# Kernel optimization log

Hardware: AMD Instinct MI355X
Metric: run time of the kernel (lower is better)

The kernel has to match this reference:

```python
import jax, jax.numpy as jnp
import numpy as np

E = 131072
MS, MV = 64, 32            # node/edge/out irreps: 64x0e + 32x1o (dim 160)
DIM = MS + 3 * MV
SC = 64                    # edge scalar dim
BETA = 1.6791767           # normalize2mom(silu) constant used by e3nn FullyConnectedNet
SQ3 = np.float32(np.sqrt(3.0))


def _split(x, ms, mv):
    # e3nn layout: [mul_s scalars | mul_v vectors (mul-major, xyz-minor)]
    return x[:, :ms], x[:, ms:].reshape(x.shape[0], mv, 3)


def _tp(xs, xv, ys, yv, Wss, Wvv, Wsv, Wvs):
    # uvw fully-connected tensor product of (m1s x0e + m1v x1o) with (1x0e + 1x1o),
    # component irrep normalization, 1/sqrt(fan_in) path weights.
    m1s, m1v = xs.shape[1], xv.shape[1]
    s_a = jnp.einsum('eu,uw->ew', xs * ys, Wss) / np.sqrt(m1s)              # 0e x 0e -> 0e
    dot = jnp.einsum('eui,ei->eu', xv, yv) / SQ3                            # 1o x 1o -> 0e
    s_b = jnp.einsum('eu,uw->ew', dot, Wvv) / np.sqrt(m1v)
    v_a = jnp.einsum('eu,ei,uw->ewi', xs, yv, Wsv) / np.sqrt(m1s)           # 0e x 1o -> 1o
    v_b = jnp.einsum('eui,uw->ewi', xv * ys[:, :, None], Wvs) / np.sqrt(m1v)  # 1o x 0e -> 1o
    return jnp.concatenate([s_a, s_b], 1), jnp.concatenate([v_a, v_b], 1)


def _mlp(x, W1, W2, W3):
    # e3nn FullyConnectedNet with silu: variance-preserving layers
    h = BETA * jax.nn.silu(x @ W1 / np.sqrt(W1.shape[0]))
    h = BETA * jax.nn.silu(h @ W2 / np.sqrt(W2.shape[0]))
    return h @ W3 / np.sqrt(W3.shape[0])


def _scale_linear(ms_, mv_, w, Wls, Wlv):
    # LinearScaleWithWeights: per-channel (uvu) scale by generated weights, then o3.Linear
    nS = ms_.shape[1]
    s = ms_ * w[:, :nS]
    v = mv_ * w[:, nS:, None]
    s2 = s @ Wls / np.sqrt(Wls.shape[0])
    v2 = jnp.einsum('eui,uw->ewi', v, Wlv) / np.sqrt(Wlv.shape[0])
    return s2, v2


def _linear(s, v, Ws, Wv):
    return s @ Ws / np.sqrt(Ws.shape[0]), jnp.einsum('eui,uw->ewi', v, Wv) / np.sqrt(Wv.shape[0])


def setup_inputs() -> dict:
    key = jax.random.key(0)
    ks = jax.random.split(key, 32)
    r = lambda i, shp: jax.random.normal(ks[i], shp, dtype=jnp.float32)
    return {
        'node_feats_src': r(0, (E, DIM)),
        'node_feats_dst': r(1, (E, DIM)),
        'edge_feats':     r(2, (E, DIM)),
        'local_env_edge': r(3, (E, 4)),
        'edge_scalars':   r(4, (E, SC)),
        # node TP (combined 128x0e+64x1o x 1x0e+1x1o -> 128x0e+64x1o)
        'Wn_ss': r(5, (2 * MS, MS)), 'Wn_vv': r(6, (2 * MV, MS)),
        'Wn_sv': r(7, (2 * MS, MV)), 'Wn_vs': r(8, (2 * MV, MV)),
        # edge TP (64x0e+32x1o x 1x0e+1x1o -> 128x0e+64x1o)
        'We_ss': r(9, (MS, MS)), 'We_vv': r(10, (MV, MS)),
        'We_sv': r(11, (MS, MV)), 'We_vs': r(12, (MV, MV)),
        # scaler output linears (128x0e+64x1o -> 64x0e+32x1o)
        'Wns_s': r(13, (2 * MS, MS)), 'Wns_v': r(14, (2 * MV, MV)),
        'Wes_s': r(15, (2 * MS, MS)), 'Wes_v': r(16, (2 * MV, MV)),
        # final output linears (irreps_out -> irreps_out)
        'Wno_s': r(17, (MS, MS)), 'Wno_v': r(18, (MV, MV)),
        'Weo_s': r(19, (MS, MS)), 'Weo_v': r(20, (MV, MV)),
        # radial MLPs [64,64,64,192]
        'Wnm1': r(21, (SC, 64)), 'Wnm2': r(22, (64, 64)), 'Wnm3': r(23, (64, 2 * MS + 2 * MV)),
        'Wem1': r(24, (SC, 64)), 'Wem2': r(25, (64, 64)), 'Wem3': r(26, (64, 2 * MS + 2 * MV)),
    }


def reference(node_feats_src, node_feats_dst, edge_feats, local_env_edge, edge_scalars,
              Wn_ss, Wn_vv, Wn_sv, Wn_vs, We_ss, We_vv, We_sv, We_vs,
              Wns_s, Wns_v, Wes_s, Wes_v, Wno_s, Wno_v, Weo_s, Weo_v,
              Wnm1, Wnm2, Wnm3, Wem1, Wem2, Wem3):
    ss, sv = _split(node_feats_src, MS, MV)
    ds, dv = _split(node_feats_dst, MS, MV)
    # AttentionHeadsToVector over stack([src,dst]): per-irrep concat -> 128x0e + 64x1o
    xs = jnp.concatenate([ss, ds], 1)
    xv = jnp.concatenate([sv, dv], 1)
    ys = local_env_edge[:, :1]
    yv = local_env_edge[:, 1:4]
    # node branch
    w_n = _mlp(edge_scalars, Wnm1, Wnm2, Wnm3)
    m_s, m_v = _tp(xs, xv, ys, yv, Wn_ss, Wn_vv, Wn_sv, Wn_vs)
    n_s, n_v = _scale_linear(m_s, m_v, w_n, Wns_s, Wns_v)
    # edge branch
    w_e = _mlp(edge_scalars, Wem1, Wem2, Wem3)
    es, ev = _split(edge_feats, MS, MV)
    e_ms, e_mv = _tp(es, ev, ys, yv, We_ss, We_vv, We_sv, We_vs)
    e_s, e_v = _scale_linear(e_ms, e_mv, w_e, Wes_s, Wes_v)
    # final linears + sum
    on_s, on_v = _linear(n_s, n_v, Wno_s, Wno_v)
    oe_s, oe_v = _linear(e_s, e_v, Weo_s, Weo_v)
    out_s = on_s + oe_s
    out_v = on_v + oe_v
    return jnp.concatenate([out_s, out_v.reshape(out_v.shape[0], -1)], 1)
```

## Files before the change

kernel.cpp:

```cpp
#include <hip/hip_runtime.h>


typedef short  bf16x8 __attribute__((ext_vector_type(8)));
typedef float  f32x4  __attribute__((ext_vector_type(4)));

constexpr float BETA  = 1.6791767f;
constexpr float RS128 = 0.088388347648318447f;
constexpr float RS64  = 0.125f;
constexpr float RS32  = 0.176776695296636881f;
constexpr float RSQ3  = 0.577350269189625842f;

enum : int {
  O_nm1 = 0,      O_nm2 = 4096,   O_nm3 = 8192,
  O_em1 = 20480,  O_em2 = 24576,  O_em3 = 28672,
  O_nss = 40960,  O_nsv = 49152,  O_nvv = 53248,  O_nvs = 57344,
  O_ess = 59392,  O_esv = 63488,  O_evv = 65536,  O_evs = 67584,
  O_nss2= 68608,  O_nsv2= 76800,  O_ess2= 78848,  O_esv2= 87040,
  O_nos = 89088,  O_nov = 93184,  O_eos = 94208,  O_eov = 98304,
  W_TOTAL = 99328
};

struct Ptrs {
  const float *src, *dst, *ef, *env, *scal;
  const ushort* wf;
  float *out;
};

struct PrepArgs {
  const float* src[22];
  int K[22], N[22], ofs[22];
  ushort* dst;
};

__device__ __forceinline__ ushort f2b(float x) {
  union { float f; unsigned u; } v; v.f = x;
  unsigned r = v.u + 0x7fffu + ((v.u >> 16) & 1u);
  return (ushort)(r >> 16);
}
__device__ __forceinline__ unsigned pk2(float a, float b) {
  unsigned r;
  asm("v_cvt_pk_bf16_f32 %0, %1, %2" : "=v"(r) : "v"(a), "v"(b));
  return r;
}
__device__ __forceinline__ float plo(unsigned p) {
  union { unsigned u; float f; } v; v.u = p << 16; return v.f;
}
__device__ __forceinline__ float phi(unsigned p) {
  union { unsigned u; float f; } v; v.u = p & 0xffff0000u; return v.f;
}

__global__ __launch_bounds__(256) void prep_kernel(PrepArgs A) {
  const int mat = blockIdx.x;
  const float* __restrict__ src = A.src[mat];
  const int K = A.K[mat], N = A.N[mat], KS = K >> 5;
  ushort* dst = A.dst + A.ofs[mat];
  const int total = (N * K) >> 3;
  for (int gi = threadIdx.x; gi < total; gi += 256) {
    int t = gi / (64 * KS), r = gi - t * 64 * KS;
    int ks = r >> 6, lane = r & 63;
    int cc = lane & 15, gg = lane >> 4;
    int n = t * 16 + cc, k0 = ks * 32 + gg * 8;
    ushort v[8];
#pragma unroll
    for (int j = 0; j < 8; ++j) v[j] = f2b(src[(size_t)(k0 + j) * N + n]);
    *(uint4*)(dst + (size_t)gi * 8) = *(const uint4*)v;
  }
}

template<int N>
__device__ __forceinline__ void lda(const ushort* __restrict__ wb, unsigned lofs, bf16x8* a) {
#pragma unroll
  for (int i = 0; i < N; ++i) a[i] = *(const bf16x8*)(wb + i * 512 + lofs);
}
template<int T, int KS>
__device__ __forceinline__ void mfm(const bf16x8* a, const bf16x8* bf, f32x4* out) {
#pragma unroll
  for (int t = 0; t < T; ++t) {
    f32x4 acc = (f32x4){0, 0, 0, 0};
#pragma unroll
    for (int ks = 0; ks < KS; ++ks)
      acc = __builtin_amdgcn_mfma_f32_16x16x32_bf16(a[t * KS + ks], bf[ks], acc, 0, 0, 0);
    out[t] = acc;
  }
}
template<int T, int KS>
__device__ __forceinline__ void mfmacc(const bf16x8* a, const bf16x8* bf, f32x4* out) {
#pragma unroll
  for (int t = 0; t < T; ++t)
#pragma unroll
    for (int ks = 0; ks < KS; ++ks)
      out[t] = __builtin_amdgcn_mfma_f32_16x16x32_bf16(a[t * KS + ks], bf[ks], out[t], 0, 0, 0);
}

__device__ __forceinline__ void put2(ushort* b, int cg, int col, const f32x4& d) {
  uint2 p; p.x = pk2(d[0], d[1]); p.y = pk2(d[2], d[3]);
  *(uint2*)(b + cg + col) = p;
}
__device__ __forceinline__ bf16x8 getf(const ushort* b, int cg, int col, int g) {
  return *(const bf16x8*)(b + cg + col + 8 * g);
}
__device__ __forceinline__ bf16x8 ldf8(const float* __restrict__ p) {
  float4 a = *(const float4*)p, b4 = *(const float4*)(p + 4);
  union { unsigned u[4]; bf16x8 v; } r;
  r.u[0] = pk2(a.x, a.y); r.u[1] = pk2(a.z, a.w);
  r.u[2] = pk2(b4.x, b4.y); r.u[3] = pk2(b4.z, b4.w);
  return r.v;
}
__device__ __forceinline__ f32x4 silu4(const f32x4& d) {
  f32x4 o;
#pragma unroll
  for (int r = 0; r < 4; ++r) { float z = d[r] * 0.125f; o[r] = BETA * z / (1.f + __expf(-z)); }
  return o;
}
__device__ __forceinline__ void vecwin(const float* __restrict__ p,
                                       float y0, float y1, float y2,
                                       bf16x8& dotf, bf16x8* xvf) {
  float v[24];
#pragma unroll
  for (int q = 0; q < 6; ++q) *(float4*)&v[4 * q] = *(const float4*)(p + 4 * q);
  float dj[8];
#pragma unroll
  for (int j = 0; j < 8; ++j)
    dj[j] = (v[3 * j] * y0 + v[3 * j + 1] * y1 + v[3 * j + 2] * y2) * RSQ3;
  union { unsigned u[4]; bf16x8 w; } t;
#pragma unroll
  for (int q = 0; q < 4; ++q) t.u[q] = pk2(dj[2 * q], dj[2 * q + 1]);
  dotf = t.w;
#pragma unroll
  for (int i = 0; i < 3; ++i) {
#pragma unroll
    for (int q = 0; q < 4; ++q) t.u[q] = pk2(v[6 * q + i], v[6 * q + 3 + i]);
    xvf[i] = t.w;
  }
}

template<bool ED>
__device__ __forceinline__ void tp_stage(
    const ushort* __restrict__ WF, ushort* b0, ushort* b1, ushort* b2,
    int cg, int g, unsigned lofs,
    const bf16x8* xsf, const bf16x8* dotf, const bf16x8* xvi,
    const uint2* Wp, float ys, float yv0, float yv1, float yv2) {
  constexpr int KA = ED ? 2 : 4;
  constexpr int KB = ED ? 1 : 2;
  const float SA = ED ? RS64 : RS128;
  const float SB = ED ? RS32 : RS64;
  const ushort* w_ss = WF + (ED ? O_ess : O_nss);
  const ushort* w_sv = WF + (ED ? O_esv : O_nsv);
  const ushort* w_vv = WF + (ED ? O_evv : O_nvv);
  const ushort* w_vs = WF + (ED ? O_evs : O_nvs);

  {
    bf16x8 a[4 * KA]; f32x4 d[4];
    lda<4 * KA>(w_ss, lofs, a); mfm<4, KA>(a, xsf, d);
#pragma unroll
    for (int t = 0; t < 4; ++t) {
      f32x4 m;
      m[0] = d[t][0] * ys * SA * plo(Wp[t].x); m[1] = d[t][1] * ys * SA * phi(Wp[t].x);
      m[2] = d[t][2] * ys * SA * plo(Wp[t].y); m[3] = d[t][3] * ys * SA * phi(Wp[t].y);
      put2(b0, cg, 16 * t + 4 * g, m);
    }
  }
  {
    bf16x8 a[4 * KB]; f32x4 d[4];
    lda<4 * KB>(w_vv, lofs, a); mfm<4, KB>(a, dotf, d);
#pragma unroll
    for (int t = 0; t < 4; ++t) {
      f32x4 m;
      m[0] = d[t][0] * SB * plo(Wp[4 + t].x); m[1] = d[t][1] * SB * phi(Wp[4 + t].x);
      m[2] = d[t][2] * SB * plo(Wp[4 + t].y); m[3] = d[t][3] * SB * phi(Wp[4 + t].y);
      put2(b0, cg, 64 + 16 * t + 4 * g, m);
    }
  }
  f32x4 ga[2];
  { bf16x8 a[2 * KA]; lda<2 * KA>(w_sv, lofs, a); mfm<2, KA>(a, xsf, ga); }
  bf16x8 avs[2 * KB];
  lda<2 * KB>(w_vs, lofs, avs);
#pragma unroll
  for (int i = 0; i < 3; ++i) {
    f32x4 db[2];
    mfm<2, KB>(avs, xvi + i * KB, db);
    float yvi = (i == 0) ? yv0 : ((i == 1) ? yv1 : yv2);
    ushort* mb = (i == 2) ? b2 : b1;
    int mbase = (i == 1) ? 64 : 0;
#pragma unroll
    for (int t = 0; t < 2; ++t) {
      f32x4 m;
      m[0] = ga[t][0] * SA * yvi * plo(Wp[8 + t].x); m[1] = ga[t][1] * SA * yvi * phi(Wp[8 + t].x);
      m[2] = ga[t][2] * SA * yvi * plo(Wp[8 + t].y); m[3] = ga[t][3] * SA * yvi * phi(Wp[8 + t].y);
      put2(mb, cg, mbase + 16 * t + 4 * g, m);
    }
#pragma unroll
    for (int t = 0; t < 2; ++t) {
      f32x4 m;
      m[0] = db[t][0] * ys * SB * plo(Wp[10 + t].x); m[1] = db[t][1] * ys * SB * phi(Wp[10 + t].x);
      m[2] = db[t][2] * ys * SB * plo(Wp[10 + t].y); m[3] = db[t][3] * ys * SB * phi(Wp[10 + t].y);
      put2(mb, cg, mbase + 32 + 16 * t + 4 * g, m);
    }
  }
}

template<bool ED>
__device__ __forceinline__ void sl_out_stage(
    const ushort* __restrict__ WF, ushort* b0, ushort* b1, ushort* b2,
    int cg, int g, unsigned lofs, f32x4* os, f32x4 (*ov)[2]) {
  const ushort* w_s2 = WF + (ED ? O_ess2 : O_nss2);
  const ushort* w_v2 = WF + (ED ? O_esv2 : O_nsv2);
  const ushort* w_os = WF + (ED ? O_eos : O_nos);
  const ushort* w_ov = WF + (ED ? O_eov : O_nov);

  bf16x8 mpf[4];
#pragma unroll
  for (int ks = 0; ks < 4; ++ks) mpf[ks] = getf(b0, cg, 32 * ks, g);
  bf16x8 mvf[6];
  mvf[0] = getf(b1, cg, 0, g);  mvf[1] = getf(b1, cg, 32, g);
  mvf[2] = getf(b1, cg, 64, g); mvf[3] = getf(b1, cg, 96, g);
  mvf[4] = getf(b2, cg, 0, g);  mvf[5] = getf(b2, cg, 32, g);
  {
    bf16x8 a[16]; f32x4 d[4];
    lda<16>(w_s2, lofs, a); mfm<4, 4>(a, mpf, d);
#pragma unroll
    for (int t = 0; t < 4; ++t) {
      f32x4 m = { d[t][0] * RS128, d[t][1] * RS128, d[t][2] * RS128, d[t][3] * RS128 };
      put2(b2, cg, 64 + 16 * t + 4 * g, m);
    }
  }
  {
    bf16x8 a[4];
    lda<4>(w_v2, lofs, a);
#pragma unroll
    for (int i = 0; i < 3; ++i) {
      f32x4 dn[2]; mfm<2, 2>(a, mvf + 2 * i, dn);
#pragma unroll
      for (int t = 0; t < 2; ++t) {
        f32x4 m = { dn[t][0] * RS64, dn[t][1] * RS64, dn[t][2] * RS64, dn[t][3] * RS64 };
        put2(b0, cg, i * 32 + 16 * t + 4 * g, m);
      }
    }
  }
  {
    bf16x8 nsf[2] = { getf(b2, cg, 64, g), getf(b2, cg, 96, g) };
    bf16x8 a[8]; lda<8>(w_os, lofs, a);
    mfmacc<4, 2>(a, nsf, os);
  }
  {
    bf16x8 a[2]; lda<2>(w_ov, lofs, a);
#pragma unroll
    for (int i = 0; i < 3; ++i) {
      bf16x8 nvf = getf(b0, cg, i * 32, g);
#pragma unroll
      for (int t = 0; t < 2; ++t)
        ov[i][t] = __builtin_amdgcn_mfma_f32_16x16x32_bf16(a[t], nvf, ov[i][t], 0, 0, 0);
    }
  }
}

__global__ __launch_bounds__(256, 3) void mp_kernel(Ptrs P) {
  const int tid  = threadIdx.x;
  const int lane = tid & 63, wid = tid >> 6;
  const int c    = lane & 15, g  = lane >> 4;
  const unsigned lofs = lane * 8;
  const int cg   = c * 136;
  const int e    = (blockIdx.x * 4 + wid) * 16 + c;
  const ushort* __restrict__ WF = P.wf;

  __shared__ ushort sb[4][3][16][136];
  ushort* b0 = &sb[wid][0][0][0];
  ushort* b1 = &sb[wid][1][0][0];
  ushort* b2 = &sb[wid][2][0][0];

  const float* __restrict__ rs = P.src + (size_t)e * 160;
  const float* __restrict__ rd = P.dst + (size_t)e * 160;
  const float* __restrict__ re = P.ef  + (size_t)e * 160;
  const float* __restrict__ rq = P.scal + (size_t)e * 64;

  float4 ev = *(const float4*)(P.env + (size_t)e * 4);
  const float ys = ev.x, yv0 = ev.y, yv1 = ev.z, yv2 = ev.w;

  bf16x8 sc[2];
  sc[0] = ldf8(rq + 8 * g);
  sc[1] = ldf8(rq + 32 + 8 * g);

  bf16x8 xsf_n[4];
  xsf_n[0] = ldf8(rs + 8 * g);  xsf_n[1] = ldf8(rs + 32 + 8 * g);
  xsf_n[2] = ldf8(rd + 8 * g);  xsf_n[3] = ldf8(rd + 32 + 8 * g);
  bf16x8 dot_n[2]; bf16x8 xv_n[6];
  {
    bf16x8 tmp[3];
    vecwin(rs + 64 + 24 * g, yv0, yv1, yv2, dot_n[0], tmp);
    xv_n[0] = tmp[0]; xv_n[2] = tmp[1]; xv_n[4] = tmp[2];
    vecwin(rd + 64 + 24 * g, yv0, yv1, yv2, dot_n[1], tmp);
    xv_n[1] = tmp[0]; xv_n[3] = tmp[1]; xv_n[5] = tmp[2];
  }

  uint2 Wpn[12], Wpe[12];
  {
    bf16x8 an[8], ae[8]; f32x4 dn[4], de[4];
    lda<8>(WF + O_nm1, lofs, an); lda<8>(WF + O_em1, lofs, ae);
    mfm<4, 2>(an, sc, dn); mfm<4, 2>(ae, sc, de);
#pragma unroll
    for (int t = 0; t < 4; ++t) put2(b0, cg, 16 * t + 4 * g, silu4(dn[t]));
#pragma unroll
    for (int t = 0; t < 4; ++t) put2(b2, cg, 16 * t + 4 * g, silu4(de[t]));
    lda<8>(WF + O_nm2, lofs, an); lda<8>(WF + O_em2, lofs, ae);
    bf16x8 hn[2] = { getf(b0, cg, 0, g), getf(b0, cg, 32, g) };
    bf16x8 he[2] = { getf(b2, cg, 0, g), getf(b2, cg, 32, g) };
    mfm<4, 2>(an, hn, dn); mfm<4, 2>(ae, he, de);
#pragma unroll
    for (int t = 0; t < 4; ++t) put2(b1, cg, 16 * t + 4 * g, silu4(dn[t]));
#pragma unroll
    for (int t = 0; t < 4; ++t) put2(b2, cg, 64 + 16 * t + 4 * g, silu4(de[t]));
    bf16x8 h2n[2] = { getf(b1, cg, 0, g), getf(b1, cg, 32, g) };
    bf16x8 h2e[2] = { getf(b2, cg, 64, g), getf(b2, cg, 96, g) };
    {
      bf16x8 a3[24]; f32x4 dw[12];
      lda<24>(WF + O_nm3, lofs, a3); mfm<12, 2>(a3, h2n, dw);
#pragma unroll
      for (int t = 0; t < 12; ++t) {
        Wpn[t].x = pk2(dw[t][0] * 0.125f, dw[t][1] * 0.125f);
        Wpn[t].y = pk2(dw[t][2] * 0.125f, dw[t][3] * 0.125f);
      }
      lda<24>(WF + O_em3, lofs, a3); mfm<12, 2>(a3, h2e, dw);
#pragma unroll
      for (int t = 0; t < 12; ++t) {
        Wpe[t].x = pk2(dw[t][0] * 0.125f, dw[t][1] * 0.125f);
        Wpe[t].y = pk2(dw[t][2] * 0.125f, dw[t][3] * 0.125f);
      }
    }
  }

  f32x4 os[4]; f32x4 ov[3][2];
#pragma unroll
  for (int t = 0; t < 4; ++t) os[t] = (f32x4){0, 0, 0, 0};
#pragma unroll
  for (int i = 0; i < 3; ++i)
#pragma unroll
    for (int t = 0; t < 2; ++t) ov[i][t] = (f32x4){0, 0, 0, 0};

  tp_stage<false>(WF, b0, b1, b2, cg, g, lofs, xsf_n, dot_n, xv_n, Wpn, ys, yv0, yv1, yv2);

  bf16x8 xsf_e[2] = { ldf8(re + 8 * g), ldf8(re + 32 + 8 * g) };
  bf16x8 dot_e[1]; bf16x8 xv_e[3];
  {
    bf16x8 tmp[3];
    vecwin(re + 64 + 24 * g, yv0, yv1, yv2, dot_e[0], tmp);
    xv_e[0] = tmp[0]; xv_e[1] = tmp[1]; xv_e[2] = tmp[2];
  }

  sl_out_stage<false>(WF, b0, b1, b2, cg, g, lofs, os, ov);

  tp_stage<true>(WF, b0, b1, b2, cg, g, lofs, xsf_e, dot_e, xv_e, Wpe, ys, yv0, yv1, yv2);
  sl_out_stage<true>(WF, b0, b1, b2, cg, g, lofs, os, ov);

  float* __restrict__ po = P.out + (size_t)e * 160;
#pragma unroll
  for (int t = 0; t < 4; ++t) {
    float4 o = { os[t][0] * RS64, os[t][1] * RS64, os[t][2] * RS64, os[t][3] * RS64 };
    *(float4*)(po + 16 * t + 4 * g) = o;
  }
#pragma unroll
  for (int t = 0; t < 2; ++t) {
    float vv[12];
#pragma unroll
    for (int r = 0; r < 4; ++r)
#pragma unroll
      for (int i = 0; i < 3; ++i) vv[3 * r + i] = ov[i][t][r] * RS32;
    *(float4*)(po + 64 + 48 * t + 12 * g)     = *(float4*)&vv[0];
    *(float4*)(po + 64 + 48 * t + 12 * g + 4) = *(float4*)&vv[4];
    *(float4*)(po + 64 + 48 * t + 12 * g + 8) = *(float4*)&vv[8];
  }
}

extern "C" void kernel_launch(void* const* d_in, const int* in_sizes, int n_in,
                              void* d_out, int out_size, void* d_ws, size_t ws_size,
                              hipStream_t stream) {
  PrepArgs A;
  const int src_idx[22] = {21,22,23, 24,25,26, 5,7,6,8, 9,11,10,12, 13,14, 15,16, 17,18, 19,20};
  const int Ks[22] = {64,64,64, 64,64,64, 128,128,64,64, 64,64,32,32, 128,64, 128,64, 64,32, 64,32};
  const int Ns[22] = {64,64,192, 64,64,192, 64,32,64,32, 64,32,64,32, 64,32, 64,32, 64,32, 64,32};
  const int Os[22] = {O_nm1,O_nm2,O_nm3, O_em1,O_em2,O_em3,
                      O_nss,O_nsv,O_nvv,O_nvs, O_ess,O_esv,O_evv,O_evs,
                      O_nss2,O_nsv2, O_ess2,O_esv2, O_nos,O_nov, O_eos,O_eov};
  for (int i = 0; i < 22; ++i) {
    A.src[i] = (const float*)d_in[src_idx[i]];
    A.K[i] = Ks[i]; A.N[i] = Ns[i]; A.ofs[i] = Os[i];
  }
  A.dst = (ushort*)d_ws;
  prep_kernel<<<dim3(22), dim3(256), 0, stream>>>(A);

  Ptrs P;
  P.src  = (const float*)d_in[0];
  P.dst  = (const float*)d_in[1];
  P.ef   = (const float*)d_in[2];
  P.env  = (const float*)d_in[3];
  P.scal = (const float*)d_in[4];
  P.wf   = (const ushort*)d_ws;
  P.out  = (float*)d_out;

  const int E = in_sizes[0] / 160;
  mp_kernel<<<dim3(E / 64), dim3(256), 0, stream>>>(P);
}
```

Baseline: 134.7 us.

## Pre-multiply scale-linear and output linear weights, shrink LDS, raise occupancy

The scale-linear o3.Linear and the following output linear are composed into one weight matrix per branch, computed by a new prep kernel with the normalisation constants folded in. This removes one GEMM stage and its LDS round trip per branch. The per-wave shared buffer becomes a single smaller padded tile, the MLP third layer is split into chunked loads, and launch bounds move from 3 to 4 blocks per SM. The risks are extra bf16 rounding from the pre-multiplied weights and register pressure under the tighter occupancy target.

```diff
diff --git a/kernel.cpp b/kernel.cpp
--- a/kernel.cpp
+++ b/kernel.cpp
@@ -3,6 +3,8 @@
 
 typedef short  bf16x8 __attribute__((ext_vector_type(8)));
 typedef float  f32x4  __attribute__((ext_vector_type(4)));
+
+#define FENCE() asm volatile("" ::: "memory")
 
 constexpr float BETA  = 1.6791767f;
 constexpr float RS128 = 0.088388347648318447f;
@@ -15,10 +17,11 @@
   O_em1 = 20480,  O_em2 = 24576,  O_em3 = 28672,
   O_nss = 40960,  O_nsv = 49152,  O_nvv = 53248,  O_nvs = 57344,
   O_ess = 59392,  O_esv = 63488,  O_evv = 65536,  O_evs = 67584,
-  O_nss2= 68608,  O_nsv2= 76800,  O_ess2= 78848,  O_esv2= 87040,
-  O_nos = 89088,  O_nov = 93184,  O_eos = 94208,  O_eov = 98304,
-  W_TOTAL = 99328
+  O_cns = 68608,  O_cnv = 76800,  O_ces = 78848,  O_cev = 87040,
+  W_TOTAL = 89088
 };
+
+enum : int { ST = 260, H0n = 0, H0e = 64, H1n = 128, H1e = 192, MSP = 0, MV = 128 };
 
 struct Ptrs {
   const float *src, *dst, *ef, *env, *scal;
@@ -27,8 +30,14 @@
 };
 
 struct PrepArgs {
-  const float* src[22];
-  int K[22], N[22], ofs[22];
+  const float* src[14];
+  int K[14], N[14], ofs[14];
+  ushort* dst;
+};
+struct Prep2Args {
+  const float* A[4]; const float* B[4];
+  int K[4], N[4], inner[4], ofs[4];
+  float scale[4];
   ushort* dst;
 };
 
@@ -67,6 +76,30 @@
   }
 }
 
+__global__ __launch_bounds__(256) void prep2_kernel(Prep2Args Z) {
+  const int m = blockIdx.x;
+  const float* __restrict__ A = Z.A[m];
+  const float* __restrict__ B = Z.B[m];
+  const int K = Z.K[m], N = Z.N[m], I = Z.inner[m], KS = K >> 5;
+  const float sc = Z.scale[m];
+  ushort* dst = Z.dst + Z.ofs[m];
+  const int total = (N * K) >> 3;
+  for (int gi = threadIdx.x; gi < total; gi += 256) {
+    int t = gi / (64 * KS), r = gi - t * 64 * KS;
+    int ks = r >> 6, lane = r & 63;
+    int cc = lane & 15, gg = lane >> 4;
+    int n = t * 16 + cc, k0 = ks * 32 + gg * 8;
+    ushort v[8];
+    for (int j = 0; j < 8; ++j) {
+      float acc = 0.f;
+      for (int u = 0; u < I; ++u)
+        acc += A[(size_t)(k0 + j) * I + u] * B[(size_t)u * N + n];
+      v[j] = f2b(acc * sc);
+    }
+    *(uint4*)(dst + (size_t)gi * 8) = *(const uint4*)v;
+  }
+}
+
 template<int N>
 __device__ __forceinline__ void lda(const ushort* __restrict__ wb, unsigned lofs, bf16x8* a) {
 #pragma unroll
@@ -134,156 +167,153 @@
   }
 }
 
-template<bool ED>
-__device__ __forceinline__ void tp_stage(
-    const ushort* __restrict__ WF, ushort* b0, ushort* b1, ushort* b2,
-    int cg, int g, unsigned lofs,
+__device__ __forceinline__ void mlp3(const ushort* __restrict__ wb, unsigned lofs,
+                                     const bf16x8* h2, uint2* Wp) {
+  bf16x8 aa[6], ab[6];
+  lda<6>(wb, lofs, aa);
+  lda<6>(wb + 6 * 512, lofs, ab);
+  f32x4 dw[3];
+  mfm<3, 2>(aa, h2, dw);
+  lda<6>(wb + 12 * 512, lofs, aa);
+#pragma unroll
+  for (int t = 0; t < 3; ++t) { Wp[t].x = pk2(dw[t][0]*0.125f, dw[t][1]*0.125f); Wp[t].y = pk2(dw[t][2]*0.125f, dw[t][3]*0.125f); }
+  mfm<3, 2>(ab, h2, dw);
+  lda<6>(wb + 18 * 512, lofs, ab);
+#pragma unroll
+  for (int t = 0; t < 3; ++t) { Wp[3+t].x = pk2(dw[t][0]*0.125f, dw[t][1]*0.125f); Wp[3+t].y = pk2(dw[t][2]*0.125f, dw[t][3]*0.125f); }
+  mfm<3, 2>(aa, h2, dw);
+#pragma unroll
+  for (int t = 0; t < 3; ++t) { Wp[6+t].x = pk2(dw[t][0]*0.125f, dw[t][1]*0.125f); Wp[6+t].y = pk2(dw[t][2]*0.125f, dw[t][3]*0.125f); }
+  mfm<3, 2>(ab, h2, dw);
+#pragma unroll
+  for (int t = 0; t < 3; ++t) { Wp[9+t].x = pk2(dw[t][0]*0.125f, dw[t][1]*0.125f); Wp[9+t].y = pk2(dw[t][2]*0.125f, dw[t][3]*0.125f); }
+}
+
+template<bool ED, bool ACC>
+__device__ __forceinline__ void tp_sl(
+    const ushort* __restrict__ WF, ushort* bA, int cg, int g, unsigned lofs,
     const bf16x8* xsf, const bf16x8* dotf, const bf16x8* xvi,
-    const uint2* Wp, float ys, float yv0, float yv1, float yv2) {
+    const uint2* Wp, float ys, float yv0, float yv1, float yv2,
+    f32x4* os, f32x4 (*ov)[2]) {
   constexpr int KA = ED ? 2 : 4;
   constexpr int KB = ED ? 1 : 2;
   const float SA = ED ? RS64 : RS128;
   const float SB = ED ? RS32 : RS64;
-  const ushort* w_ss = WF + (ED ? O_ess : O_nss);
-  const ushort* w_sv = WF + (ED ? O_esv : O_nsv);
-  const ushort* w_vv = WF + (ED ? O_evv : O_nvv);
-  const ushort* w_vs = WF + (ED ? O_evs : O_nvs);
 
   {
     bf16x8 a[4 * KA]; f32x4 d[4];
-    lda<4 * KA>(w_ss, lofs, a); mfm<4, KA>(a, xsf, d);
+    lda<4 * KA>(WF + (ED ? O_ess : O_nss), lofs, a);
+    mfm<4, KA>(a, xsf, d);
 #pragma unroll
     for (int t = 0; t < 4; ++t) {
       f32x4 m;
-      m[0] = d[t][0] * ys * SA * plo(Wp[t].x); m[1] = d[t][1] * ys * SA * phi(Wp[t].x);
-      m[2] = d[t][2] * ys * SA * plo(Wp[t].y); m[3] = d[t][3] * ys * SA * phi(Wp[t].y);
-      put2(b0, cg, 16 * t + 4 * g, m);
+      m[0] = d[t][0]*ys*SA*plo(Wp[t].x); m[1] = d[t][1]*ys*SA*phi(Wp[t].x);
+      m[2] = d[t][2]*ys*SA*plo(Wp[t].y); m[3] = d[t][3]*ys*SA*phi(Wp[t].y);
+      put2(bA, cg, MSP + 16 * t + 4 * g, m);
     }
   }
   {
     bf16x8 a[4 * KB]; f32x4 d[4];
-    lda<4 * KB>(w_vv, lofs, a); mfm<4, KB>(a, dotf, d);
+    lda<4 * KB>(WF + (ED ? O_evv : O_nvv), lofs, a);
+    mfm<4, KB>(a, dotf, d);
 #pragma unroll
     for (int t = 0; t < 4; ++t) {
       f32x4 m;
-      m[0] = d[t][0] * SB * plo(Wp[4 + t].x); m[1] = d[t][1] * SB * phi(Wp[4 + t].x);
-      m[2] = d[t][2] * SB * plo(Wp[4 + t].y); m[3] = d[t][3] * SB * phi(Wp[4 + t].y);
-      put2(b0, cg, 64 + 16 * t + 4 * g, m);
+      m[0] = d[t][0]*SB*plo(Wp[4+t].x); m[1] = d[t][1]*SB*phi(Wp[4+t].x);
+      m[2] = d[t][2]*SB*plo(Wp[4+t].y); m[3] = d[t][3]*SB*phi(Wp[4+t].y);
+      put2(bA, cg, MSP + 64 + 16 * t + 4 * g, m);
     }
   }
+  FENCE();
+  bf16x8 mpf[4];
+#pragma unroll
+  for (int ks = 0; ks < 4; ++ks) mpf[ks] = getf(bA, cg, MSP + 32 * ks, g);
+  bf16x8 acs[16];
+  lda<16>(WF + (ED ? O_ces : O_cns), lofs, acs);
+
   f32x4 ga[2];
-  { bf16x8 a[2 * KA]; lda<2 * KA>(w_sv, lofs, a); mfm<2, KA>(a, xsf, ga); }
+  {
+    bf16x8 a[2 * KA];
+    lda<2 * KA>(WF + (ED ? O_esv : O_nsv), lofs, a);
+    mfm<2, KA>(a, xsf, ga);
+  }
   bf16x8 avs[2 * KB];
-  lda<2 * KB>(w_vs, lofs, avs);
+  lda<2 * KB>(WF + (ED ? O_evs : O_nvs), lofs, avs);
+  bf16x8 acv[4];
+  lda<4>(WF + (ED ? O_cev : O_cnv), lofs, acv);
 #pragma unroll
   for (int i = 0; i < 3; ++i) {
     f32x4 db[2];
     mfm<2, KB>(avs, xvi + i * KB, db);
     float yvi = (i == 0) ? yv0 : ((i == 1) ? yv1 : yv2);
-    ushort* mb = (i == 2) ? b2 : b1;
-    int mbase = (i == 1) ? 64 : 0;
 #pragma unroll
     for (int t = 0; t < 2; ++t) {
       f32x4 m;
-      m[0] = ga[t][0] * SA * yvi * plo(Wp[8 + t].x); m[1] = ga[t][1] * SA * yvi * phi(Wp[8 + t].x);
-      m[2] = ga[t][2] * SA * yvi * plo(Wp[8 + t].y); m[3] = ga[t][3] * SA * yvi * phi(Wp[8 + t].y);
-      put2(mb, cg, mbase + 16 * t + 4 * g, m);
+      m[0] = ga[t][0]*SA*yvi*plo(Wp[8+t].x); m[1] = ga[t][1]*SA*yvi*phi(Wp[8+t].x);
+      m[2] = ga[t][2]*SA*yvi*plo(Wp[8+t].y); m[3] = ga[t][3]*SA*yvi*phi(Wp[8+t].y);
+      put2(bA, cg, MV + 16 * t + 4 * g, m);
     }
 #pragma unroll
     for (int t = 0; t < 2; ++t) {
       f32x4 m;
-      m[0] = db[t][0] * ys * SB * plo(Wp[10 + t].x); m[1] = db[t][1] * ys * SB * phi(Wp[10 + t].x);
-      m[2] = db[t][2] * ys * SB * plo(Wp[10 + t].y); m[3] = db[t][3] * ys * SB * phi(Wp[10 + t].y);
-      put2(mb, cg, mbase + 32 + 16 * t + 4 * g, m);
+      m[0] = db[t][0]*ys*SB*plo(Wp[10+t].x); m[1] = db[t][1]*ys*SB*phi(Wp[10+t].x);
+      m[2] = db[t][2]*ys*SB*plo(Wp[10+t].y); m[3] = db[t][3]*ys*SB*phi(Wp[10+t].y);
+      put2(bA, cg, MV + 32 + 16 * t + 4 * g, m);
     }
-  }
-}
-
-template<bool ED>
-__device__ __forceinline__ void sl_out_stage(
-    const ushort* __restrict__ WF, ushort* b0, ushort* b1, ushort* b2,
-    int cg, int g, unsigned lofs, f32x4* os, f32x4 (*ov)[2]) {
-  const ushort* w_s2 = WF + (ED ? O_ess2 : O_nss2);
-  const ushort* w_v2 = WF + (ED ? O_esv2 : O_nsv2);
-  const ushort* w_os = WF + (ED ? O_eos : O_nos);
-  const ushort* w_ov = WF + (ED ? O_eov : O_nov);
-
-  bf16x8 mpf[4];
-#pragma unroll
-  for (int ks = 0; ks < 4; ++ks) mpf[ks] = getf(b0, cg, 32 * ks, g);
-  bf16x8 mvf[6];
-  mvf[0] = getf(b1, cg, 0, g);  mvf[1] = getf(b1, cg, 32, g);
-  mvf[2] = getf(b1, cg, 64, g); mvf[3] = getf(b1, cg, 96, g);
-  mvf[4] = getf(b2, cg, 0, g);  mvf[5] = getf(b2, cg, 32, g);
-  {
-    bf16x8 a[16]; f32x4 d[4];
-    lda<16>(w_s2, lofs, a); mfm<4, 4>(a, mpf, d);
-#pragma unroll
-    for (int t = 0; t < 4; ++t) {
-      f32x4 m = { d[t][0] * RS128, d[t][1] * RS128, d[t][2] * RS128, d[t][3] * RS128 };
-      put2(b2, cg, 64 + 16 * t + 4 * g, m);
-    }
-  }
-  {
-    bf16x8 a[4];
-    lda<4>(w_v2, lofs, a);
-#pragma unroll
-    for (int i = 0; i < 3; ++i) {
-      f32x4 dn[2]; mfm<2, 2>(a, mvf + 2 * i, dn);
-#pragma unroll
-      for (int t = 0; t < 2; ++t) {
-        f32x4 m = { dn[t][0] * RS64, dn[t][1] * RS64, dn[t][2] * RS64, dn[t][3] * RS64 };
-        put2(b0, cg, i * 32 + 16 * t + 4 * g, m);
-      }
-    }
-  }
-  {
-    bf16x8 nsf[2] = { getf(b2, cg, 64, g), getf(b2, cg, 96, g) };
-    bf16x8 a[8]; lda<8>(w_os, lofs, a);
-    mfmacc<4, 2>(a, nsf, os);
-  }
-  {
-    bf16x8 a[2]; lda<2>(w_ov, lofs, a);
-#pragma unroll
-    for (int i = 0; i < 3; ++i) {
-      bf16x8 nvf = getf(b0, cg, i * 32, g);
-#pragma unroll
-      for (int t = 0; t < 2; ++t)
-        ov[i][t] = __builtin_amdgcn_mfma_f32_16x16x32_bf16(a[t], nvf, ov[i][t], 0, 0, 0);
-    }
-  }
-}
-
-__global__ __launch_bounds__(256, 3) void mp_kernel(Ptrs P) {
+    FENCE();
+    bf16x8 mvf[2] = { getf(bA, cg, MV, g), getf(bA, cg, MV + 32, g) };
+    if (ACC) mfmacc<2, 2>(acv, mvf, ov[i]);
+    else     mfm<2, 2>(acv, mvf, ov[i]);
+    FENCE();
+  }
+  if (ACC) mfmacc<4, 4>(acs, mpf, os);
+  else     mfm<4, 4>(acs, mpf, os);
+}
+
+__global__ __launch_bounds__(256, 4) void mp_kernel(Ptrs P) {
   const int tid  = threadIdx.x;
   const int lane = tid & 63, wid = tid >> 6;
   const int c    = lane & 15, g  = lane >> 4;
   const unsigned lofs = lane * 8;
-  const int cg   = c * 136;
+  const int cg   = c * ST;
   const int e    = (blockIdx.x * 4 + wid) * 16 + c;
   const ushort* __restrict__ WF = P.wf;
 
-  __shared__ ushort sb[4][3][16][136];
-  ushort* b0 = &sb[wid][0][0][0];
-  ushort* b1 = &sb[wid][1][0][0];
-  ushort* b2 = &sb[wid][2][0][0];
+  __shared__ ushort sb[4][16][ST];
+  ushort* bA = &sb[wid][0][0];
 
   const float* __restrict__ rs = P.src + (size_t)e * 160;
   const float* __restrict__ rd = P.dst + (size_t)e * 160;
   const float* __restrict__ re = P.ef  + (size_t)e * 160;
   const float* __restrict__ rq = P.scal + (size_t)e * 64;
 
+  bf16x8 a1n[8], a1e[8];
+  lda<8>(WF + O_nm1, lofs, a1n);
+  lda<8>(WF + O_em1, lofs, a1e);
+
   float4 ev = *(const float4*)(P.env + (size_t)e * 4);
   const float ys = ev.x, yv0 = ev.y, yv1 = ev.z, yv2 = ev.w;
-
   bf16x8 sc[2];
   sc[0] = ldf8(rq + 8 * g);
   sc[1] = ldf8(rq + 32 + 8 * g);
 
+  {
+    f32x4 dn[4], de[4];
+    mfm<4, 2>(a1n, sc, dn); mfm<4, 2>(a1e, sc, de);
+#pragma unroll
+    for (int t = 0; t < 4; ++t) put2(bA, cg, H0n + 16 * t + 4 * g, silu4(dn[t]));
+#pragma unroll
+    for (int t = 0; t < 4; ++t) put2(bA, cg, H0e + 16 * t + 4 * g, silu4(de[t]));
+  }
+  FENCE();
+
+  bf16x8 a2n[8], a2e[8];
+  lda<8>(WF + O_nm2, lofs, a2n);
+  lda<8>(WF + O_em2, lofs, a2e);
   bf16x8 xsf_n[4];
   xsf_n[0] = ldf8(rs + 8 * g);  xsf_n[1] = ldf8(rs + 32 + 8 * g);
   xsf_n[2] = ldf8(rd + 8 * g);  xsf_n[3] = ldf8(rd + 32 + 8 * g);
-  bf16x8 dot_n[2]; bf16x8 xv_n[6];
+  bf16x8 dot_n[2], xv_n[6];
   {
     bf16x8 tmp[3];
     vecwin(rs + 64 + 24 * g, yv0, yv1, yv2, dot_n[0], tmp);
@@ -291,70 +321,48 @@
     vecwin(rd + 64 + 24 * g, yv0, yv1, yv2, dot_n[1], tmp);
     xv_n[1] = tmp[0]; xv_n[3] = tmp[1]; xv_n[5] = tmp[2];
   }
-
-  uint2 Wpn[12], Wpe[12];
-  {
-    bf16x8 an[8], ae[8]; f32x4 dn[4], de[4];
-    lda<8>(WF + O_nm1, lofs, an); lda<8>(WF + O_em1, lofs, ae);
-    mfm<4, 2>(an, sc, dn); mfm<4, 2>(ae, sc, de);
-#pragma unroll
-    for (int t = 0; t < 4; ++t) put2(b0, cg, 16 * t + 4 * g, silu4(dn[t]));
-#pragma unroll
-    for (int t = 0; t < 4; ++t) put2(b2, cg, 16 * t + 4 * g, silu4(de[t]));
-    lda<8>(WF + O_nm2, lofs, an); lda<8>(WF + O_em2, lofs, ae);
-    bf16x8 hn[2] = { getf(b0, cg, 0, g), getf(b0, cg, 32, g) };
-    bf16x8 he[2] = { getf(b2, cg, 0, g), getf(b2, cg, 32, g) };
-    mfm<4, 2>(an, hn, dn); mfm<4, 2>(ae, he, de);
-#pragma unroll
-    for (int t = 0; t < 4; ++t) put2(b1, cg, 16 * t + 4 * g, silu4(dn[t]));
-#pragma unroll
-    for (int t = 0; t < 4; ++t) put2(b2, cg, 64 + 16 * t + 4 * g, silu4(de[t]));
-    bf16x8 h2n[2] = { getf(b1, cg, 0, g), getf(b1, cg, 32, g) };
-    bf16x8 h2e[2] = { getf(b2, cg, 64, g), getf(b2, cg, 96, g) };
-    {
-      bf16x8 a3[24]; f32x4 dw[12];
-      lda<24>(WF + O_nm3, lofs, a3); mfm<12, 2>(a3, h2n, dw);
-#pragma unroll
-      for (int t = 0; t < 12; ++t) {
-        Wpn[t].x = pk2(dw[t][0] * 0.125f, dw[t][1] * 0.125f);
-        Wpn[t].y = pk2(dw[t][2] * 0.125f, dw[t][3] * 0.125f);
-      }
-      lda<24>(WF + O_em3, lofs, a3); mfm<12, 2>(a3, h2e, dw);
-#pragma unroll
-      for (int t = 0; t < 12; ++t) {
-        Wpe[t].x = pk2(dw[t][0] * 0.125f, dw[t][1] * 0.125f);
-        Wpe[t].y = pk2(dw[t][2] * 0.125f, dw[t][3] * 0.125f);
-      }
-    }
-  }
+  {
+    bf16x8 hn[2] = { getf(bA, cg, H0n, g), getf(bA, cg, H0n + 32, g) };
+    bf16x8 he[2] = { getf(bA, cg, H0e, g), getf(bA, cg, H0e + 32, g) };
+    f32x4 dn[4], de[4];
+    mfm<4, 2>(a2n, hn, dn); mfm<4, 2>(a2e, he, de);
+#pragma unroll
+    for (int t = 0; t < 4; ++t) put2(bA, cg, H1n + 16 * t + 4 * g, silu4(dn[t]));
+#pragma unroll
+    for (int t = 0; t < 4; ++t) put2(bA, cg, H1e + 16 * t + 4 * g, silu4(de[t]));
+  }
+  FENCE();
+
+  uint2 Wpn[12];
+  {
+    bf16x8 h2n[2] = { getf(bA, cg, H1n, g), getf(bA, cg, H1n + 32, g) };
+    mlp3(WF + O_nm3, lofs, h2n, Wpn);
+  }
+  FENCE();
 
   f32x4 os[4]; f32x4 ov[3][2];
-#pragma unroll
-  for (int t = 0; t < 4; ++t) os[t] = (f32x4){0, 0, 0, 0};
-#pragma unroll
-  for (int i = 0; i < 3; ++i)
-#pragma unroll
-    for (int t = 0; t < 2; ++t) ov[i][t] = (f32x4){0, 0, 0, 0};
-
-  tp_stage<false>(WF, b0, b1, b2, cg, g, lofs, xsf_n, dot_n, xv_n, Wpn, ys, yv0, yv1, yv2);
-
-  bf16x8 xsf_e[2] = { ldf8(re + 8 * g), ldf8(re + 32 + 8 * g) };
-  bf16x8 dot_e[1]; bf16x8 xv_e[3];
+  tp_sl<false, false>(WF, bA, cg, g, lofs, xsf_n, dot_n, xv_n, Wpn, ys, yv0, yv1, yv2, os, ov);
+
+  bf16x8 xsf_e[2], dot_e[1], xv_e[3];
+  xsf_e[0] = ldf8(re + 8 * g); xsf_e[1] = ldf8(re + 32 + 8 * g);
   {
     bf16x8 tmp[3];
     vecwin(re + 64 + 24 * g, yv0, yv1, yv2, dot_e[0], tmp);
     xv_e[0] = tmp[0]; xv_e[1] = tmp[1]; xv_e[2] = tmp[2];
   }
-
-  sl_out_stage<false>(WF, b0, b1, b2, cg, g, lofs, os, ov);
-
-  tp_stage<true>(WF, b0, b1, b2, cg, g, lofs, xsf_e, dot_e, xv_e, Wpe, ys, yv0, yv1, yv2);
-  sl_out_stage<true>(WF, b0, b1, b2, cg, g, lofs, os, ov);
+  uint2 Wpe[12];
+  {
+    bf16x8 h2e[2] = { getf(bA, cg, H1e, g), getf(bA, cg, H1e + 32, g) };
+    mlp3(WF + O_em3, lofs, h2e, Wpe);
+  }
+  FENCE();
+
+  tp_sl<true, true>(WF, bA, cg, g, lofs, xsf_e, dot_e, xv_e, Wpe, ys, yv0, yv1, yv2, os, ov);
 
   float* __restrict__ po = P.out + (size_t)e * 160;
 #pragma unroll
   for (int t = 0; t < 4; ++t) {
-    float4 o = { os[t][0] * RS64, os[t][1] * RS64, os[t][2] * RS64, os[t][3] * RS64 };
+    float4 o = { os[t][0], os[t][1], os[t][2], os[t][3] };
     *(float4*)(po + 16 * t + 4 * g) = o;
   }
 #pragma unroll
@@ -363,7 +371,7 @@
 #pragma unroll
     for (int r = 0; r < 4; ++r)
 #pragma unroll
-      for (int i = 0; i < 3; ++i) vv[3 * r + i] = ov[i][t][r] * RS32;
+      for (int i = 0; i < 3; ++i) vv[3 * r + i] = ov[i][t][r];
     *(float4*)(po + 64 + 48 * t + 12 * g)     = *(float4*)&vv[0];
     *(float4*)(po + 64 + 48 * t + 12 * g + 4) = *(float4*)&vv[4];
     *(float4*)(po + 64 + 48 * t + 12 * g + 8) = *(float4*)&vv[8];
@@ -374,18 +382,29 @@
                               void* d_out, int out_size, void* d_ws, size_t ws_size,
                               hipStream_t stream) {
   PrepArgs A;
-  const int src_idx[22] = {21,22,23, 24,25,26, 5,7,6,8, 9,11,10,12, 13,14, 15,16, 17,18, 19,20};
-  const int Ks[22] = {64,64,64, 64,64,64, 128,128,64,64, 64,64,32,32, 128,64, 128,64, 64,32, 64,32};
-  const int Ns[22] = {64,64,192, 64,64,192, 64,32,64,32, 64,32,64,32, 64,32, 64,32, 64,32, 64,32};
-  const int Os[22] = {O_nm1,O_nm2,O_nm3, O_em1,O_em2,O_em3,
-                      O_nss,O_nsv,O_nvv,O_nvs, O_ess,O_esv,O_evv,O_evs,
-                      O_nss2,O_nsv2, O_ess2,O_esv2, O_nos,O_nov, O_eos,O_eov};
-  for (int i = 0; i < 22; ++i) {
+  const int src_idx[14] = {21,22,23, 24,25,26, 5,7,6,8, 9,11,10,12};
+  const int Ks[14] = {64,64,64, 64,64,64, 128,128,64,64, 64,64,32,32};
+  const int Ns[14] = {64,64,192, 64,64,192, 64,32,64,32, 64,32,64,32};
+  const int Os[14] = {O_nm1,O_nm2,O_nm3, O_em1,O_em2,O_em3,
+                      O_nss,O_nsv,O_nvv,O_nvs, O_ess,O_esv,O_evv,O_evs};
+  for (int i = 0; i < 14; ++i) {
     A.src[i] = (const float*)d_in[src_idx[i]];
     A.K[i] = Ks[i]; A.N[i] = Ns[i]; A.ofs[i] = Os[i];
   }
   A.dst = (ushort*)d_ws;
-  prep_kernel<<<dim3(22), dim3(256), 0, stream>>>(A);
+  prep_kernel<<<dim3(14), dim3(256), 0, stream>>>(A);
+
+  Prep2Args Z;
+  Z.A[0] = (const float*)d_in[13]; Z.B[0] = (const float*)d_in[17];
+  Z.K[0] = 128; Z.N[0] = 64; Z.inner[0] = 64; Z.ofs[0] = O_cns; Z.scale[0] = RS128 * RS64;
+  Z.A[1] = (const float*)d_in[14]; Z.B[1] = (const float*)d_in[18];
+  Z.K[1] = 64;  Z.N[1] = 32; Z.inner[1] = 32; Z.ofs[1] = O_cnv; Z.scale[1] = RS64 * RS32;
+  Z.A[2] = (const float*)d_in[15]; Z.B[2] = (const float*)d_in[19];
+  Z.K[2] = 128; Z.N[2] = 64; Z.inner[2] = 64; Z.ofs[2] = O_ces; Z.scale[2] = RS128 * RS64;
+  Z.A[3] = (const float*)d_in[16]; Z.B[3] = (const float*)d_in[20];
+  Z.K[3] = 64;  Z.N[3] = 32; Z.inner[3] = 32; Z.ofs[3] = O_cev; Z.scale[3] = RS64 * RS32;
+  Z.dst = (ushort*)d_ws;
+  prep2_kernel<<<dim3(4), dim3(256), 0, stream>>>(Z);
 
   Ptrs P;
   P.src  = (const float*)d_in[0];
```

Measured after the change: 416.7 us. 3.09x slower.
